# Optimization experiments

Hardware: AMD Instinct MI355X
Metric: run time of the kernel (lower is better)

## Reference

```python
import jax, jax.numpy as jnp
import numpy as np

DIM = 2048
N_HEADS = 16
Q_LORA = 1536
KV_LORA = 512
NOPE = 128
ROPE = 64
V_DIM = 128
QK_HEAD = NOPE + ROPE
SEQ = 4096
THETA = 10000.0
EPS = 1e-6
SCALE = QK_HEAD ** -0.5  # max_seq_len==4096 not >4096, so no mscale adjustment


def rms_norm(x, w):
    return x * jax.lax.rsqrt(jnp.mean(x * x, axis=-1, keepdims=True) + EPS) * w


def rope_cos_sin(seqlen):
    inv_freq = 1.0 / THETA ** (jnp.arange(0, ROPE, 2, dtype=jnp.float32) / ROPE)  # [ROPE/2]
    t = jnp.arange(seqlen, dtype=jnp.float32)
    freqs = jnp.outer(t, inv_freq)  # [S, ROPE/2]
    return jnp.cos(freqs), jnp.sin(freqs)


def apply_rope(x, cos, sin):
    # x: (b, s, h, ROPE); pairs (x0, x1) rotated as complex mult, interleaved layout
    b, s, h, d = x.shape
    xr = x.reshape(b, s, h, d // 2, 2)
    x0, x1 = xr[..., 0], xr[..., 1]
    c = cos[None, :, None, :]
    sn = sin[None, :, None, :]
    out = jnp.stack([x0 * c - x1 * sn, x0 * sn + x1 * c], axis=-1)
    return out.reshape(b, s, h, d)


def setup_inputs() -> dict:
    key = jax.random.key(0)
    ks = jax.random.split(key, 8)
    s = lambda fan_in: 1.0 / np.sqrt(fan_in)
    return {
        "x": jax.random.normal(ks[0], (1, SEQ, DIM), jnp.float32),
        "wq_a_w": jax.random.normal(ks[1], (Q_LORA, DIM), jnp.float32) * s(DIM),
        "q_norm_w": 1.0 + 0.02 * jax.random.normal(ks[2], (Q_LORA,), jnp.float32),
        "wq_b_w": jax.random.normal(ks[3], (N_HEADS * QK_HEAD, Q_LORA), jnp.float32) * s(Q_LORA),
        "wkv_a_w": jax.random.normal(ks[4], (KV_LORA + ROPE, DIM), jnp.float32) * s(DIM),
        "kv_norm_w": 1.0 + 0.02 * jax.random.normal(ks[5], (KV_LORA,), jnp.float32),
        "wkv_b_w": jax.random.normal(ks[6], (N_HEADS * (NOPE + V_DIM), KV_LORA), jnp.float32) * s(KV_LORA),
        "wo_w": jax.random.normal(ks[7], (DIM, DIM), jnp.float32) * s(DIM),
    }


def reference(x, wq_a_w, q_norm_w, wq_b_w, wkv_a_w, kv_norm_w, wkv_b_w, wo_w):
    b, seqlen, _ = x.shape
    cos, sin = rope_cos_sin(seqlen)

    # Q path: low-rank down-proj -> RMSNorm -> up-proj
    q = rms_norm(x @ wq_a_w.T, q_norm_w) @ wq_b_w.T
    q = q.reshape(b, seqlen, N_HEADS, QK_HEAD)
    q_nope, q_pe = q[..., :NOPE], q[..., NOPE:]
    q_pe = apply_rope(q_pe, cos, sin)

    # KV path: compressed latent + decoupled rope key
    kv_a = x @ wkv_a_w.T  # (b, s, KV_LORA + ROPE)
    kv_latent, k_pe_raw = kv_a[..., :KV_LORA], kv_a[..., KV_LORA:]
    kv = rms_norm(kv_latent, kv_norm_w)               # (b, t, c)
    k_pe = apply_rope(k_pe_raw[:, :, None, :], cos, sin)[:, :, 0, :]  # (b, t, r)

    # Absorption trick: fold wkv_b's K-part into q_nope, attend against latents
    wkv_b = wkv_b_w.reshape(N_HEADS, NOPE + V_DIM, KV_LORA)
    q_abs = jnp.einsum("bshd,hdc->bshc", q_nope, wkv_b[:, :NOPE])

    scores = (jnp.einsum("bshc,btc->bsht", q_abs, kv)
              + jnp.einsum("bshr,btr->bsht", q_pe, k_pe)) * SCALE

    # causal additive mask over (s_query, t_key)
    causal = jnp.tril(jnp.ones((seqlen, seqlen), dtype=bool))
    scores = jnp.where(causal[None, :, None, :], scores, jnp.float32(-1e30))
    attn = jax.nn.softmax(scores, axis=-1)

    # post-softmax: aggregate latents, then recover V via wkv_b's V-part
    ctx = jnp.einsum("bsht,btc->bshc", attn, kv)
    v = jnp.einsum("bshc,hdc->bshd", ctx, wkv_b[:, NOPE:])  # (b, s, h, V_DIM)
    out = v.reshape(b, seqlen, N_HEADS * V_DIM) @ wo_w.T
    return out
```

## Files before the change

### kernel.cpp

```cpp
#include <hip/hip_runtime.h>

typedef unsigned short u16;
typedef __attribute__((ext_vector_type(8))) short bf16x8;
typedef __attribute__((ext_vector_type(4))) float f32x4;
typedef __attribute__((ext_vector_type(4))) unsigned short u16x4;

#define MFMA16(a, b, c) __builtin_amdgcn_mfma_f32_16x16x32_bf16((a), (b), (c), 0, 0, 0)

#define SEQ 4096
#define SCALE 0.07216878364870323f
#define LOGTHETA 9.210340371976184f

__device__ __forceinline__ u16 f2bf(float f) {
  union { float f; unsigned u; } c; c.f = f;
  unsigned u = c.u;
  unsigned r = (u + 0x7fffu + ((u >> 16) & 1u)) >> 16;
  return (u16)r;
}
__device__ __forceinline__ float bf2f(u16 b) {
  union { unsigned u; float f; } c; c.u = ((unsigned)b) << 16;
  return c.f;
}

__global__ void cvt_bf16(const float* __restrict__ src, u16* __restrict__ dst, int n4) {
  int stride = gridDim.x * blockDim.x;
  for (int i = blockIdx.x * blockDim.x + threadIdx.x; i < n4; i += stride) {
    f32x4 v = ((const f32x4*)src)[i];
    u16x4 o;
    o[0] = f2bf(v[0]); o[1] = f2bf(v[1]); o[2] = f2bf(v[2]); o[3] = f2bf(v[3]);
    ((u16x4*)dst)[i] = o;
  }
}

__global__ void trans_wkvb(const u16* __restrict__ w, u16* __restrict__ wt) {
  int stride = gridDim.x * blockDim.x;
  for (int i = blockIdx.x * blockDim.x + threadIdx.x; i < 16 * 512 * 128; i += stride) {
    int h = i >> 16;
    int r = i & 65535;
    int c = r >> 7, d = r & 127;
    wt[i] = w[(h * 256 + d) * 512 + c];
  }
}

__global__ void trans_vt(const u16* __restrict__ kva, u16* __restrict__ vt2) {
  __shared__ u16 tile[64][65];
  int c0 = blockIdx.x * 64;
  int t0 = blockIdx.y * 64;
  for (int k = 0; k < 16; k++) {
    int el = threadIdx.x + k * 256;
    int r = el >> 6, c = el & 63;
    tile[r][c] = kva[(t0 + r) * 576 + c0 + c];
  }
  __syncthreads();
  for (int k = 0; k < 16; k++) {
    int el = threadIdx.x + k * 256;
    int r = el >> 6, c = el & 63;
    int t = t0 + c;
    vt2[(t >> 5) * 16384 + (c0 + r) * 32 + (t & 31)] = tile[c][r];
  }
}

__global__ void rms_q_kernel(u16* __restrict__ qa, const float* __restrict__ w) {
  int row = blockIdx.x;
  u16* p = qa + row * 1536;
  float vals[6];
  float ss = 0.f;
#pragma unroll
  for (int k = 0; k < 6; k++) {
    float v = bf2f(p[threadIdx.x + k * 256]);
    vals[k] = v;
    ss += v * v;
  }
  for (int m = 1; m < 64; m <<= 1) ss += __shfl_xor(ss, m);
  __shared__ float red[4];
  int wid = threadIdx.x >> 6;
  if ((threadIdx.x & 63) == 0) red[wid] = ss;
  __syncthreads();
  float tot = red[0] + red[1] + red[2] + red[3];
  float rr = rsqrtf(tot / 1536.f + 1e-6f);
#pragma unroll
  for (int k = 0; k < 6; k++) {
    int i = threadIdx.x + k * 256;
    p[i] = f2bf(vals[k] * rr * w[i]);
  }
}

__global__ void rms_kv_kernel(u16* __restrict__ kva, const float* __restrict__ w) {
  int t = blockIdx.x;
  u16* p = kva + t * 576;
  float v0 = bf2f(p[threadIdx.x]);
  float v1 = bf2f(p[threadIdx.x + 256]);
  float ss = v0 * v0 + v1 * v1;
  for (int m = 1; m < 64; m <<= 1) ss += __shfl_xor(ss, m);
  __shared__ float red[4];
  int wid = threadIdx.x >> 6;
  if ((threadIdx.x & 63) == 0) red[wid] = ss;
  __syncthreads();
  float tot = red[0] + red[1] + red[2] + red[3];
  float rr = rsqrtf(tot / 512.f + 1e-6f);
  p[threadIdx.x] = f2bf(v0 * rr * w[threadIdx.x]);
  p[threadIdx.x + 256] = f2bf(v1 * rr * w[threadIdx.x + 256]);
  if (threadIdx.x < 32) {
    int i = threadIdx.x;
    float x0 = bf2f(p[512 + 2 * i]);
    float x1 = bf2f(p[512 + 2 * i + 1]);
    float invf = expf(-((float)(2 * i) / 64.f) * LOGTHETA);
    float ang = (float)t * invf;
    float cs = cosf(ang), sn = sinf(ang);
    p[512 + 2 * i] = f2bf(x0 * cs - x1 * sn);
    p[512 + 2 * i + 1] = f2bf(x0 * sn + x1 * cs);
  }
}

__global__ void rope_q_kernel(const u16* __restrict__ qb, u16* __restrict__ qcat) {
  int stride = gridDim.x * blockDim.x;
  for (int idx = blockIdx.x * blockDim.x + threadIdx.x; idx < 4096 * 512; idx += stride) {
    int s = idx >> 9;
    int r = idx & 511;
    int h = r >> 5, i = r & 31;
    float x0 = bf2f(qb[s * 3072 + h * 192 + 128 + 2 * i]);
    float x1 = bf2f(qb[s * 3072 + h * 192 + 128 + 2 * i + 1]);
    float invf = expf(-((float)(2 * i) / 64.f) * LOGTHETA);
    float ang = (float)s * invf;
    float cs = cosf(ang) * SCALE, sn = sinf(ang) * SCALE;
    qcat[s * 9216 + h * 576 + 512 + 2 * i] = f2bf(x0 * cs - x1 * sn);
    qcat[s * 9216 + h * 576 + 512 + 2 * i + 1] = f2bf(x0 * sn + x1 * cs);
  }
}

template <int BN, bool OUTF32>
__launch_bounds__(256)
__global__ void gemm_tiled(const u16* __restrict__ A, int lda, int az,
                           const u16* __restrict__ W, int ldw, int wz,
                           void* __restrict__ Cp, int ldc, int cz, int K, float oscale) {
  constexpr int NCH = 8 + BN / 16;
  constexpr int NBF = BN / 32;
  __shared__ __align__(16) u16 lds[2][NCH * 512];

  int z = blockIdx.z;
  int wid = threadIdx.x >> 6, lane = threadIdx.x & 63;
  int quad = lane >> 4, l16 = lane & 15;
  int wr = wid >> 1, wc = wid & 1;
  int m0 = blockIdx.y * 128;
  int n0 = blockIdx.x * BN;

  const u16* Az = A + (size_t)z * az;
  const u16* Wz = W + (size_t)z * wz;

  f32x4 acc[4][NBF];
#pragma unroll
  for (int i = 0; i < 4; i++)
#pragma unroll
    for (int j = 0; j < NBF; j++) acc[i][j] = {0.f, 0.f, 0.f, 0.f};

#pragma unroll
  for (int jj = 0; jj < NCH / 4; jj++) {
    int c = jj * 4 + wid;
    const u16* src = (c < 8) ? (Az + (m0 + c * 16 + l16) * (size_t)lda + quad * 8)
                             : (Wz + (n0 + (c - 8) * 16 + l16) * (size_t)ldw + quad * 8);
    __builtin_amdgcn_global_load_lds(
        (const __attribute__((address_space(1))) unsigned int*)src,
        (__attribute__((address_space(3))) unsigned int*)&lds[0][c * 512], 16, 0, 0);
  }

  int buf = 0;
  for (int k0 = 0; k0 < K; k0 += 32) {
    __syncthreads();
    if (k0 + 32 < K) {
      int k1 = k0 + 32;
#pragma unroll
      for (int jj = 0; jj < NCH / 4; jj++) {
        int c = jj * 4 + wid;
        const u16* src = (c < 8) ? (Az + (m0 + c * 16 + l16) * (size_t)lda + k1 + quad * 8)
                                 : (Wz + (n0 + (c - 8) * 16 + l16) * (size_t)ldw + k1 + quad * 8);
        __builtin_amdgcn_global_load_lds(
            (const __attribute__((address_space(1))) unsigned int*)src,
            (__attribute__((address_space(3))) unsigned int*)&lds[buf ^ 1][c * 512], 16, 0, 0);
      }
    }
    const u16* base = &lds[buf][0];
    bf16x8 a[4], b[NBF];
#pragma unroll
    for (int i = 0; i < 4; i++)
      a[i] = *(const bf16x8*)(base + (wr * 4 + i) * 512 + lane * 8);
#pragma unroll
    for (int j = 0; j < NBF; j++)
      b[j] = *(const bf16x8*)(base + (8 + wc * NBF + j) * 512 + lane * 8);
#pragma unroll
    for (int i = 0; i < 4; i++)
#pragma unroll
      for (int j = 0; j < NBF; j++) acc[i][j] = MFMA16(a[i], b[j], acc[i][j]);
    buf ^= 1;
  }

#pragma unroll
  for (int i = 0; i < 4; i++) {
    int row = m0 + wr * 64 + i * 16 + quad * 4;
#pragma unroll
    for (int j = 0; j < NBF; j++) {
      int col = n0 + wc * (BN / 2) + j * 16 + l16;
#pragma unroll
      for (int r = 0; r < 4; r++) {
        size_t cbase = (size_t)z * cz + (size_t)(row + r) * ldc + col;
        if (OUTF32) ((float*)Cp)[cbase] = acc[i][j][r] * oscale;
        else        ((u16*)Cp)[cbase] = f2bf(acc[i][j][r] * oscale);
      }
    }
  }
}

__launch_bounds__(512, 2)
__global__ void attn_kernel(const u16* __restrict__ qcat, const u16* __restrict__ kcat,
                            const u16* __restrict__ vt2, u16* __restrict__ ctx) {
  __shared__ __align__(16) u16 lds[2][34816];
  __shared__ __align__(16) u16 plds[8][16][40];

  int wid = threadIdx.x >> 6, lane = threadIdx.x & 63;
  int quad = lane >> 4, l16 = lane & 15;
  int bx = blockIdx.x;
  int h = bx & 15;
  int jb = 31 - (bx >> 4);
  int qb0 = jb << 7;
  int m0 = qb0 + wid * 16;

  bf16x8 q[18];
  {
    const u16* qb = qcat + (m0 + l16) * 9216 + h * 576 + quad * 8;
#pragma unroll
    for (int kk = 0; kk < 18; kk++) q[kk] = *(const bf16x8*)(qb + kk * 32);
  }

  f32x4 zero = {0.f, 0.f, 0.f, 0.f};
  f32x4 o[32];
#pragma unroll
  for (int ct = 0; ct < 32; ct++) o[ct] = zero;
  float li[4] = {0.f, 0.f, 0.f, 0.f};

  int nt = (qb0 >> 5) + 4;

  const u16* sp[9];
  int sstr[9], soff[9];
  bool sact[9];
#pragma unroll
  for (int jj = 0; jj < 9; jj++) {
    int c = jj * 8 + wid;
    sact[jj] = (c < 68);
    soff[jj] = c * 512;
    if (c < 36) {
      int kk = c >> 1, half = c & 1;
      sp[jj] = kcat + (half * 16 + l16) * 576 + kk * 32 + quad * 8;
      sstr[jj] = 32 * 576;
    } else {
      int ct = c - 36;
      sp[jj] = vt2 + (ct * 16 + l16) * 32 + quad * 8;
      sstr[jj] = 16384;
    }
  }

#pragma unroll
  for (int jj = 0; jj < 9; jj++) {
    if (sact[jj]) {
      __builtin_amdgcn_global_load_lds(
          (const __attribute__((address_space(1))) unsigned int*)sp[jj],
          (__attribute__((address_space(3))) unsigned int*)&lds[0][soff[jj]], 16, 0, 0);
      sp[jj] += sstr[jj];
    }
  }

  for (int ti = 0; ti < nt; ti++) {
    __syncthreads();
    int buf = ti & 1;
    if (ti + 1 < nt) {
      u16* dbase = &lds[buf ^ 1][0];
#pragma unroll
      for (int jj = 0; jj < 9; jj++) {
        if (sact[jj]) {
          __builtin_amdgcn_global_load_lds(
              (const __attribute__((address_space(1))) unsigned int*)sp[jj],
              (__attribute__((address_space(3))) unsigned int*)&dbase[soff[jj]], 16, 0, 0);
          sp[jj] += sstr[jj];
        }
      }
    }

    int t0 = ti << 5;
    if (t0 <= m0 + 15) {
      const u16* kb = &lds[buf][0];
      const u16* vb = &lds[buf][18432];
      f32x4 s0 = zero, s1 = zero;
#pragma unroll
      for (int kk = 0; kk < 18; kk++) {
        bf16x8 b0 = *(const bf16x8*)(&kb[(kk * 2 + 0) * 512 + lane * 8]);
        bf16x8 b1 = *(const bf16x8*)(&kb[(kk * 2 + 1) * 512 + lane * 8]);
        s0 = MFMA16(q[kk], b0, s0);
        s1 = MFMA16(q[kk], b1, s1);
      }
      int tc0 = t0 + l16, tc1 = t0 + 16 + l16;
#pragma unroll
      for (int r = 0; r < 4; r++) {
        int mrow = m0 + quad * 4 + r;
        float e0 = (tc0 <= mrow) ? __expf(s0[r]) : 0.f;
        float e1 = (tc1 <= mrow) ? __expf(s1[r]) : 0.f;
        li[r] += e0 + e1;
        plds[wid][quad * 4 + r][l16] = f2bf(e0);
        plds[wid][quad * 4 + r][16 + l16] = f2bf(e1);
      }
      __threadfence_block();
      bf16x8 ap = *(const bf16x8*)(&plds[wid][l16][quad * 8]);
#pragma unroll
      for (int ct = 0; ct < 32; ct++) {
        bf16x8 bv = *(const bf16x8*)(&vb[ct * 512 + lane * 8]);
        o[ct] = MFMA16(ap, bv, o[ct]);
      }
    }
  }

#pragma unroll
  for (int r = 0; r < 4; r++) {
    float s = li[r];
    s += __shfl_xor(s, 1);
    s += __shfl_xor(s, 2);
    s += __shfl_xor(s, 4);
    s += __shfl_xor(s, 8);
    li[r] = s;
  }
  f32x4 inv = {1.f / li[0], 1.f / li[1], 1.f / li[2], 1.f / li[3]};
#pragma unroll
  for (int ct = 0; ct < 32; ct++) {
    f32x4 val = o[ct] * inv;
    int base = (m0 + quad * 4) * 8192 + h * 512 + ct * 16 + l16;
    ctx[base] = f2bf(val[0]);
    ctx[base + 8192] = f2bf(val[1]);
    ctx[base + 2 * 8192] = f2bf(val[2]);
    ctx[base + 3 * 8192] = f2bf(val[3]);
  }
}

extern "C" void kernel_launch(void* const* d_in, const int* in_sizes, int n_in,
                              void* d_out, int out_size, void* d_ws, size_t ws_size,
                              hipStream_t stream) {
  const float* x = (const float*)d_in[0];
  const float* wqa = (const float*)d_in[1];
  const float* qnw = (const float*)d_in[2];
  const float* wqb = (const float*)d_in[3];
  const float* wkva = (const float*)d_in[4];
  const float* kvnw = (const float*)d_in[5];
  const float* wkvb = (const float*)d_in[6];
  const float* wo = (const float*)d_in[7];

  u16* ws = (u16*)d_ws;
  u16* XB = ws;
  u16* WQAB = ws + 8388608;
  u16* WQBB = ws + 11534336;
  u16* WKVAB = ws + 16252928;
  u16* WKVBB = ws + 17432576;
  u16* WKVBT = ws + 19529728;
  u16* WOB = ws + 20578304;
  u16* QA = ws + 24772608;
  u16* KVA = ws + 31064064;
  u16* VT = ws + 33423360;
  u16* QCAT = ws + 35520512;
  u16* CTX = ws + 73269248;
  u16* QB = CTX;
  u16* VBUF = QCAT;

  dim3 blk(256);

  cvt_bf16<<<1024, blk, 0, stream>>>(x, XB, 2097152);
  cvt_bf16<<<1024, blk, 0, stream>>>(wqa, WQAB, 786432);
  cvt_bf16<<<1024, blk, 0, stream>>>(wqb, WQBB, 1179648);
  cvt_bf16<<<1024, blk, 0, stream>>>(wkva, WKVAB, 294912);
  cvt_bf16<<<1024, blk, 0, stream>>>(wkvb, WKVBB, 524288);
  cvt_bf16<<<1024, blk, 0, stream>>>(wo, WOB, 1048576);
  trans_wkvb<<<1024, blk, 0, stream>>>(WKVBB, WKVBT);

  gemm_tiled<128, false><<<dim3(12, 32, 1), blk, 0, stream>>>(XB, 2048, 0, WQAB, 2048, 0, QA, 1536, 0, 2048, 1.f);
  gemm_tiled<64, false><<<dim3(9, 32, 1), blk, 0, stream>>>(XB, 2048, 0, WKVAB, 2048, 0, KVA, 576, 0, 2048, 1.f);

  rms_q_kernel<<<4096, blk, 0, stream>>>(QA, qnw);
  rms_kv_kernel<<<4096, blk, 0, stream>>>(KVA, kvnw);
  trans_vt<<<dim3(8, 64), blk, 0, stream>>>(KVA, VT);

  gemm_tiled<128, false><<<dim3(24, 32, 1), blk, 0, stream>>>(QA, 1536, 0, WQBB, 1536, 0, QB, 3072, 0, 1536, 1.f);

  gemm_tiled<128, false><<<dim3(4, 32, 16), blk, 0, stream>>>(QB, 3072, 192, WKVBT, 128, 65536, QCAT, 9216, 576, 128, SCALE);
  rope_q_kernel<<<2048, blk, 0, stream>>>(QB, QCAT);

  attn_kernel<<<512, dim3(512), 0, stream>>>(QCAT, KVA, VT, CTX);

  gemm_tiled<128, false><<<dim3(1, 32, 16), blk, 0, stream>>>(CTX, 8192, 512, WKVBB + 65536, 512, 131072, VBUF, 2048, 128, 512, 1.f);

  gemm_tiled<128, true><<<dim3(16, 32, 1), blk, 0, stream>>>(VBUF, 2048, 0, WOB, 2048, 0, d_out, 2048, 0, 2048, 1.f);
}
```

Before: 925.4 us.

## Split PV matmul across waves as 64-row by 128-column tiles with shared P

Before, each wave computed its own 16-row by 512-column P·V product, reading all 32 V fragments from LDS per tile. Now the waves publish their P tiles to LDS, synchronise, and each wave computes a 64x128 output block (4 row tiles by 8 column tiles). Each V fragment read is reused across four MFMAs, cutting LDS traffic for V. The cost is an extra block-wide barrier per key tile, waves whose rows are fully masked writing zeros, and a row-sum exchange through LDS before the final normalisation.

```diff
diff --git a/kernel.cpp b/kernel.cpp
--- a/kernel.cpp
+++ b/kernel.cpp
@@ -213,7 +213,8 @@
 __global__ void attn_kernel(const u16* __restrict__ qcat, const u16* __restrict__ kcat,
                             const u16* __restrict__ vt2, u16* __restrict__ ctx) {
   __shared__ __align__(16) u16 lds[2][34816];
-  __shared__ __align__(16) u16 plds[8][16][40];
+  __shared__ __align__(16) u16 plds[8][512];
+  __shared__ float li_lds[128];
 
   int wid = threadIdx.x >> 6, lane = threadIdx.x & 63;
   int quad = lane >> 4, l16 = lane & 15;
@@ -222,6 +223,8 @@
   int jb = 31 - (bx >> 4);
   int qb0 = jb << 7;
   int m0 = qb0 + wid * 16;
+  int rg = wid >> 2, ch = wid & 3;
+  int pr0 = rg * 64;
 
   bf16x8 q[18];
   {
@@ -231,9 +234,10 @@
   }
 
   f32x4 zero = {0.f, 0.f, 0.f, 0.f};
+  bf16x8 zero8 = {0, 0, 0, 0, 0, 0, 0, 0};
   f32x4 o[32];
 #pragma unroll
-  for (int ct = 0; ct < 32; ct++) o[ct] = zero;
+  for (int k = 0; k < 32; k++) o[k] = zero;
   float li[4] = {0.f, 0.f, 0.f, 0.f};
 
   int nt = (qb0 >> 5) + 4;
@@ -286,7 +290,6 @@
     int t0 = ti << 5;
     if (t0 <= m0 + 15) {
       const u16* kb = &lds[buf][0];
-      const u16* vb = &lds[buf][18432];
       f32x4 s0 = zero, s1 = zero;
 #pragma unroll
       for (int kk = 0; kk < 18; kk++) {
@@ -302,15 +305,26 @@
         float e0 = (tc0 <= mrow) ? __expf(s0[r]) : 0.f;
         float e1 = (tc1 <= mrow) ? __expf(s1[r]) : 0.f;
         li[r] += e0 + e1;
-        plds[wid][quad * 4 + r][l16] = f2bf(e0);
-        plds[wid][quad * 4 + r][16 + l16] = f2bf(e1);
-      }
-      __threadfence_block();
-      bf16x8 ap = *(const bf16x8*)(&plds[wid][l16][quad * 8]);
-#pragma unroll
-      for (int ct = 0; ct < 32; ct++) {
-        bf16x8 bv = *(const bf16x8*)(&vb[ct * 512 + lane * 8]);
-        o[ct] = MFMA16(ap, bv, o[ct]);
+        int row = quad * 4 + r;
+        plds[wid][((l16 >> 3) * 16 + row) * 8 + (l16 & 7)] = f2bf(e0);
+        plds[wid][((2 + (l16 >> 3)) * 16 + row) * 8 + (l16 & 7)] = f2bf(e1);
+      }
+    } else {
+      *(bf16x8*)&plds[wid][lane * 8] = zero8;
+    }
+    __syncthreads();
+
+    if (t0 <= qb0 + pr0 + 63) {
+      const u16* vb = &lds[buf][18432];
+      bf16x8 a[4];
+#pragma unroll
+      for (int i = 0; i < 4; i++)
+        a[i] = *(const bf16x8*)(&plds[rg * 4 + i][lane * 8]);
+#pragma unroll
+      for (int j = 0; j < 8; j++) {
+        bf16x8 bv = *(const bf16x8*)(&vb[(ch * 8 + j) * 512 + lane * 8]);
+#pragma unroll
+        for (int i = 0; i < 4; i++) o[i * 8 + j] = MFMA16(a[i], bv, o[i * 8 + j]);
       }
     }
   }
@@ -324,15 +338,26 @@
     s += __shfl_xor(s, 8);
     li[r] = s;
   }
-  f32x4 inv = {1.f / li[0], 1.f / li[1], 1.f / li[2], 1.f / li[3]};
-#pragma unroll
-  for (int ct = 0; ct < 32; ct++) {
-    f32x4 val = o[ct] * inv;
-    int base = (m0 + quad * 4) * 8192 + h * 512 + ct * 16 + l16;
-    ctx[base] = f2bf(val[0]);
-    ctx[base + 8192] = f2bf(val[1]);
-    ctx[base + 2 * 8192] = f2bf(val[2]);
-    ctx[base + 3 * 8192] = f2bf(val[3]);
+  if (l16 == 0) {
+#pragma unroll
+    for (int r = 0; r < 4; r++) li_lds[wid * 16 + quad * 4 + r] = li[r];
+  }
+  __syncthreads();
+#pragma unroll
+  for (int i = 0; i < 4; i++) {
+    int rowl = pr0 + i * 16 + quad * 4;
+    f32x4 inv;
+#pragma unroll
+    for (int r = 0; r < 4; r++) inv[r] = 1.f / li_lds[rowl + r];
+    int grow = qb0 + rowl;
+#pragma unroll
+    for (int j = 0; j < 8; j++) {
+      int col = ch * 128 + j * 16 + l16;
+      f32x4 val = o[i * 8 + j] * inv;
+#pragma unroll
+      for (int r = 0; r < 4; r++)
+        ctx[(size_t)(grow + r) * 8192 + h * 512 + col] = f2bf(val[r]);
+    }
   }
 }
 
```

Result: slower. 993.5 us (+7.4%).
